# Optimization experiments

Hardware: AMD Instinct MI355X
Metric: run time of the kernel (lower is better)

Reference implementation:

```python
import math
import jax, jax.numpy as jnp
import numpy as np
from jax import lax

N, L = 256, 4096
DIM_LINEAR, DIM_CONV, KERNEL, STRIDE = 64, 128, 15, 1


def setup_inputs() -> dict:
    key = jax.random.key(0)
    ks = jax.random.split(key, 10)
    tokens = jax.random.randint(ks[0], (N, L), 0, 4, dtype=jnp.int32)
    emb = jax.random.normal(ks[1], (4, DIM_LINEAR), dtype=jnp.float32)
    conv_w = jax.random.normal(ks[2], (DIM_CONV, DIM_LINEAR, KERNEL), dtype=jnp.float32) * (1.0 / math.sqrt(DIM_LINEAR * KERNEL))
    conv_b = jax.random.normal(ks[3], (DIM_CONV,), dtype=jnp.float32) * 0.01
    s = 1.0 / math.sqrt(DIM_CONV)
    Wq = jax.random.normal(ks[4], (DIM_CONV, DIM_CONV), dtype=jnp.float32) * s
    bq = jax.random.normal(ks[5], (DIM_CONV,), dtype=jnp.float32) * 0.01
    Wk = jax.random.normal(ks[6], (DIM_CONV, DIM_CONV), dtype=jnp.float32) * s
    bk = jax.random.normal(ks[7], (DIM_CONV,), dtype=jnp.float32) * 0.01
    Wv = jax.random.normal(ks[8], (DIM_CONV, DIM_CONV), dtype=jnp.float32) * s
    bv = jax.random.normal(ks[9], (DIM_CONV,), dtype=jnp.float32) * 0.01
    return {"tokens": tokens, "emb": emb, "conv_w": conv_w, "conv_b": conv_b,
            "Wq": Wq, "bq": bq, "Wk": Wk, "bk": bk, "Wv": Wv, "bv": bv}


def reference(tokens, emb, conv_w, conv_b, Wq, bq, Wk, bk, Wv, bv):
    # embedding: [N, L, dl] -> channels-first [N, dl, L]
    x = emb[tokens].transpose(0, 2, 1)
    # conv1d, valid padding: [N, dc, Lout]
    y = lax.conv_general_dilated(x, conv_w, window_strides=(STRIDE,),
                                 padding='VALID',
                                 dimension_numbers=('NCH', 'OIH', 'NCH'))
    y = y + conv_b[None, :, None]
    read = y.transpose(0, 2, 1)                      # [N, Lout, dc]
    read_mean = read.mean(axis=1)                    # [N, dc]
    q = read_mean @ Wq.T + bq                        # [N, dc]
    k = read @ Wk.T + bk                             # [N, Lout, dc]
    v = read @ Wv.T + bv                             # [N, Lout, dc]
    scores = jnp.einsum('nd,nld->nl', q, k) / math.sqrt(DIM_CONV)
    attn = jax.nn.softmax(scores, axis=1)            # [N, Lout]
    out = jnp.einsum('nl,nld->nd', attn, v)          # [N, dc]
    return out
```

## Files before the change

### kernel.cpp

```cpp
#include <hip/hip_runtime.h>
#include <math.h>

#define NN 256
#define LL 4096
#define DL 64
#define DC 128
#define KS 15
#define LOUT (LL - KS + 1)
#define RSQRT_DC 0.08838834764831843f
#define INV_LOUT (1.0f / (float)LOUT)

#define WS_CTB   0
#define WS_QC    7680
#define WS_KC    15360
#define WS_G     23040
#define WS_S0    30720
#define WS_BB    30784
#define WS_B0    30848
#define WS_OUTB  30976
#define WS_PACK  31104
#define WS_CNT   96640

__global__ __launch_bounds__(256) void prep1_kernel(const int* __restrict__ tokens,
                                                    const float* __restrict__ emb,
                                                    const float* __restrict__ conv_w,
                                                    float* __restrict__ ws) {
    const int b = blockIdx.x, tid = threadIdx.x;
    if (b < NN) {
        __shared__ int totw[4][4];
        const int n = b;
        const int4* tv = (const int4*)(tokens + (size_t)n * LL) + tid * 4;
        unsigned w = 0;
#pragma unroll
        for (int m = 0; m < 4; ++m) {
            int4 t4 = tv[m];
            w |= ((unsigned)t4.x | ((unsigned)t4.y << 2) |
                  ((unsigned)t4.z << 4) | ((unsigned)t4.w << 6)) << (8 * m);
        }
        ((unsigned*)ws)[WS_PACK + n * 256 + tid] = w;
        int c0, c1, c2, c3;
        unsigned y, z;
        y = w;               z = (y | (y >> 1)) & 0x55555555u; c0 = 16 - __popc(z);
        y = w ^ 0x55555555u; z = (y | (y >> 1)) & 0x55555555u; c1 = 16 - __popc(z);
        y = w ^ 0xAAAAAAAAu; z = (y | (y >> 1)) & 0x55555555u; c2 = 16 - __popc(z);
        y = w ^ 0xFFFFFFFFu; z = (y | (y >> 1)) & 0x55555555u; c3 = 16 - __popc(z);
#pragma unroll
        for (int off = 32; off > 0; off >>= 1) {
            c0 += __shfl_down(c0, off, 64); c1 += __shfl_down(c1, off, 64);
            c2 += __shfl_down(c2, off, 64); c3 += __shfl_down(c3, off, 64);
        }
        if ((tid & 63) == 0) {
            const int wv = tid >> 6;
            totw[wv][0] = c0; totw[wv][1] = c1; totw[wv][2] = c2; totw[wv][3] = c3;
        }
        __syncthreads();
        if (tid < 4)
            ((int*)ws)[WS_CNT + n * 4 + tid] =
                totw[0][tid] + totw[1][tid] + totw[2][tid] + totw[3][tid];
    } else {
        const int c = b - NN;
        __shared__ float wsm[DL][16];
        __shared__ float es[4][DL];
        const float* wsrc = conv_w + (size_t)c * (DL * KS);
        for (int idx = tid; idx < DL * KS; idx += 256) wsm[idx / KS][idx % KS] = wsrc[idx];
        es[tid >> 6][tid & 63] = emb[tid];
        __syncthreads();
        if (tid < 60) {
            const int v = tid / KS, k = tid % KS;
            float s = 0.f;
#pragma unroll
            for (int i = 0; i < DL; ++i) s += es[v][i] * wsm[i][k];
            ws[WS_CTB + tid * DC + c] = s;
        }
    }
}

__global__ __launch_bounds__(128) void prep2_kernel(
    const float* __restrict__ conv_b,
    const float* __restrict__ Wq, const float* __restrict__ bq,
    const float* __restrict__ Wk, const float* __restrict__ bk,
    const float* __restrict__ Wv, const float* __restrict__ bv,
    float* __restrict__ ws) {
    const int j = blockIdx.x, c = threadIdx.x;
    __shared__ float cbL[DC];
    __shared__ float red2a[2], red2b[2];
    cbL[c] = conv_b[c];
    if (j < 60) {
        __shared__ float ctbj[DC];
        ctbj[c] = ws[WS_CTB + j * DC + c];
        __syncthreads();
        const float4* wq = (const float4*)(Wq + (size_t)c * DC);
        const float4* wk = (const float4*)(Wk + (size_t)c * DC);
        const float4* wv = (const float4*)(Wv + (size_t)c * DC);
        const float4* ct4 = (const float4*)ctbj;
        const float4* cb4 = (const float4*)cbL;
        float qc = 0.f, q0c = 0.f, kc = 0.f, kcbc = 0.f, gc = 0.f;
#pragma unroll 8
        for (int t = 0; t < 32; ++t) {
            const float4 a = wq[t], b = wk[t], g = wv[t], x = ct4[t], y = cb4[t];
            qc   += a.x * x.x + a.y * x.y + a.z * x.z + a.w * x.w;
            q0c  += a.x * y.x + a.y * y.y + a.z * y.z + a.w * y.w;
            kc   += b.x * x.x + b.y * x.y + b.z * x.z + b.w * x.w;
            kcbc += b.x * y.x + b.y * y.y + b.z * y.z + b.w * y.w;
            gc   += g.x * x.x + g.y * x.y + g.z * x.z + g.w * x.w;
        }
        ws[WS_QC + j * DC + c] = qc;
        ws[WS_KC + j * DC + c] = kc;
        ws[WS_G  + j * DC + c] = gc;
        const float beta = kcbc + bk[c];
        q0c += bq[c];
        float t1 = kc * q0c;
        float t2 = qc * beta;
#pragma unroll
        for (int off = 32; off > 0; off >>= 1) {
            t1 += __shfl_down(t1, off, 64);
            t2 += __shfl_down(t2, off, 64);
        }
        if ((c & 63) == 0) { red2a[c >> 6] = t1; red2b[c >> 6] = t2; }
        __syncthreads();
        if (c == 0) {
            ws[WS_S0 + j] = (red2a[0] + red2a[1]) * RSQRT_DC;
            ws[WS_BB + j] = (red2b[0] + red2b[1]) * RSQRT_DC;
        }
    } else {
        __syncthreads();
        const float4* wq = (const float4*)(Wq + (size_t)c * DC);
        const float4* wk = (const float4*)(Wk + (size_t)c * DC);
        const float4* wv = (const float4*)(Wv + (size_t)c * DC);
        const float4* cb4 = (const float4*)cbL;
        float q0c = 0.f, kcbc = 0.f, ob = 0.f;
#pragma unroll 8
        for (int t = 0; t < 32; ++t) {
            const float4 a = wq[t], b = wk[t], g = wv[t], y = cb4[t];
            q0c  += a.x * y.x + a.y * y.y + a.z * y.z + a.w * y.w;
            kcbc += b.x * y.x + b.y * y.y + b.z * y.z + b.w * y.w;
            ob   += g.x * y.x + g.y * y.y + g.z * y.z + g.w * y.w;
        }
        ws[WS_OUTB + c] = ob + bv[c];
        q0c += bq[c];
        float t1 = q0c * (kcbc + bk[c]);
#pragma unroll
        for (int off = 32; off > 0; off >>= 1) t1 += __shfl_down(t1, off, 64);
        if ((c & 63) == 0) red2a[c >> 6] = t1;
        __syncthreads();
        if (c == 0) ws[WS_B0] = (red2a[0] + red2a[1]) * RSQRT_DC;
    }
}

template <int NW>
__device__ __forceinline__ float bsum(float v, float* red, int tid) {
#pragma unroll
    for (int off = 32; off > 0; off >>= 1) v += __shfl_down(v, off, 64);
    if ((tid & 63) == 0) red[tid >> 6] = v;
    __syncthreads();
    float r = 0.f;
#pragma unroll
    for (int w = 0; w < NW; ++w) r += red[w];
    __syncthreads();
    return r;
}

__global__ __launch_bounds__(512) void encode_kernel(
    const float* __restrict__ ws, float* __restrict__ out) {
    const int n = blockIdx.x, tid = threadIdx.x;
    const unsigned* packed = (const unsigned*)ws + WS_PACK;

    __shared__ unsigned tok2L[258];
    __shared__ float stabL[64];
    __shared__ float cfL[60];
    __shared__ float uL[DC];
    __shared__ float Tt[1024];
    __shared__ float AccL[45];
    __shared__ float red[8];

    if (tid >= 64) {
        const int i = tid - 64;
        if (i < 258) tok2L[i] = (i < 256) ? packed[n * 256 + i] : 0u;
        else if (i < 258 + 45) AccL[i - 258] = 0.f;
    } else {
        const int l = tid;
        const int4 ct = *(const int4*)((const int*)ws + WS_CNT + n * 4);
        const unsigned dwF = packed[n * 256];
        const unsigned dwL = packed[n * 256 + 255];
        if (l < KS) {
            const int k = l;
            const unsigned pm = (k == 0) ? 0u : ((1u << (2 * k)) - 1u);
            const unsigned sm = (k == 14) ? 0u : (0xFFFFFFFFu << (2 * (k + 2)));
            const int tot4[4] = {ct.x, ct.y, ct.z, ct.w};
#pragma unroll
            for (int v = 0; v < 4; ++v) {
                const unsigned patt = (unsigned)v * 0x55555555u;
                unsigned yf = dwF ^ patt, zf = (yf | (yf >> 1)) & 0x55555555u;
                unsigned yl = dwL ^ patt, zl = (yl | (yl >> 1)) & 0x55555555u;
                const int pre = k - __popc(zf & pm);
                const int suf = (14 - k) - __popc(zl & sm);
                cfL[v * KS + k] = (float)(tot4[v] - pre - suf) * INV_LOUT;
            }
        }
        const int c0 = 2 * l;
        float u0 = 0.f, u1 = 0.f;
        for (int j = 0; j < 60; ++j) {
            const float cfj = cfL[j];
            const float2 q2 = *(const float2*)(ws + WS_QC + j * DC + c0);
            u0 += cfj * q2.x; u1 += cfj * q2.y;
        }
        uL[c0] = u0; uL[c0 + 1] = u1;
        float t = (l < 60) ? cfL[l] * ws[WS_BB + l] : 0.f;
#pragma unroll
        for (int off = 32; off > 0; off >>= 1) t += __shfl_down(t, off, 64);
        if (l == 0) stabL[60] = ws[WS_B0] + t;
        if (l < 60) {
            const float4* kr = (const float4*)(ws + WS_KC + (size_t)l * DC);
            const float4* u4 = (const float4*)uL;
            float s = 0.f;
#pragma unroll 8
            for (int t2 = 0; t2 < 32; ++t2) {
                const float4 a = kr[t2], u = u4[t2];
                s += a.x * u.x + a.y * u.y + a.z * u.z + a.w * u.w;
            }
            stabL[l] = ws[WS_S0 + l] + s * RSQRT_DC;
        }
    }
    __syncthreads();

    const float base = stabL[60];
    for (int e = tid; e < 1024; e += 512) {
        const int j = e >> 8, bb = e & 255;
        float s = stabL[(bb & 3) * KS + 4 * j] +
                  stabL[((bb >> 2) & 3) * KS + 4 * j + 1] +
                  stabL[((bb >> 4) & 3) * KS + 4 * j + 2];
        if (j < 3) s += stabL[((bb >> 6) & 3) * KS + 4 * j + 3];
        Tt[e] = s;
    }
    float M = base;
#pragma unroll
    for (int k = 0; k < KS; ++k)
        M += fmaxf(fmaxf(stabL[k], stabL[KS + k]),
                   fmaxf(stabL[2 * KS + k], stabL[3 * KS + k]));
    __syncthreads();

    const unsigned d0 = tok2L[tid >> 1], d1 = tok2L[(tid >> 1) + 1];
    const unsigned long long W = (unsigned long long)d0 | ((unsigned long long)d1 << 32);
    const int sbase = (tid & 1) << 4;
    const int t0 = tid * 8;
    float ev[8];
    float lsum = 0.f;
#pragma unroll
    for (int p = 0; p < 8; ++p) {
        const unsigned w = (unsigned)(W >> (sbase + 2 * p));
        const float s = base + Tt[w & 255] + Tt[256 + ((w >> 8) & 255)] +
                        Tt[512 + ((w >> 16) & 255)] + Tt[768 + ((w >> 24) & 63)];
        const float e = (t0 + p < LOUT) ? __expf(s - M) : 0.f;
        ev[p] = e; lsum += e;
    }
    const float S = bsum<8>(lsum, red, tid);
    const float invS = 1.0f / S;

    float a1[KS], a2[KS], a3[KS];
#pragma unroll
    for (int k = 0; k < KS; ++k) { a1[k] = 0.f; a2[k] = 0.f; a3[k] = 0.f; }
#pragma unroll
    for (int p = 0; p < 8; ++p) {
        const float e = ev[p];
        const unsigned w = (unsigned)(W >> (sbase + 2 * p));
#pragma unroll
        for (int k = 0; k < KS; ++k) {
            const int v = (int)((w >> (2 * k)) & 3u);
            a1[k] += (v == 1) ? e : 0.f;
            a2[k] += (v == 2) ? e : 0.f;
            a3[k] += (v == 3) ? e : 0.f;
        }
    }
    {
        const int lane = tid & 63;
#pragma unroll
        for (int k = 0; k < KS; ++k) {
            float v1 = a1[k], v2 = a2[k], v3 = a3[k];
#pragma unroll
            for (int off = 32; off > 0; off >>= 1) {
                v1 += __shfl_down(v1, off, 64);
                v2 += __shfl_down(v2, off, 64);
                v3 += __shfl_down(v3, off, 64);
            }
            if (lane == 0) {
                atomicAdd(&AccL[k], v1);
                atomicAdd(&AccL[KS + k], v2);
                atomicAdd(&AccL[2 * KS + k], v3);
            }
        }
    }
    __syncthreads();

    if (tid < DC) {
        float s = 0.f;
#pragma unroll
        for (int k = 0; k < KS; ++k) {
            const float a0 = S - AccL[k] - AccL[KS + k] - AccL[2 * KS + k];
            s += a0 * ws[WS_G + k * DC + tid];
        }
#pragma unroll
        for (int j = KS; j < 60; ++j) s += AccL[j - KS] * ws[WS_G + j * DC + tid];
        out[(size_t)n * DC + tid] = ws[WS_OUTB + tid] + s * invS;
    }
}

extern "C" void kernel_launch(void* const* d_in, const int* in_sizes, int n_in,
                              void* d_out, int out_size, void* d_ws, size_t ws_size,
                              hipStream_t stream) {
    const int*   tokens = (const int*)d_in[0];
    const float* emb    = (const float*)d_in[1];
    const float* conv_w = (const float*)d_in[2];
    const float* conv_b = (const float*)d_in[3];
    const float* Wq     = (const float*)d_in[4];
    const float* bq     = (const float*)d_in[5];
    const float* Wk     = (const float*)d_in[6];
    const float* bk     = (const float*)d_in[7];
    const float* Wv     = (const float*)d_in[8];
    const float* bv     = (const float*)d_in[9];
    float* out = (float*)d_out;
    float* ws  = (float*)d_ws;

    prep1_kernel<<<NN + DC, 256, 0, stream>>>(tokens, emb, conv_w, ws);
    prep2_kernel<<<61, 128, 0, stream>>>(conv_b, Wq, bq, Wk, bk, Wv, bv, ws);
    encode_kernel<<<NN, 512, 0, stream>>>(ws, out);
}
```

Measured before the change: 104.8 us.

## Fold token packing into encode kernel and merge weight prep into one kernel

Moves token packing and per-sequence token counting from a separate prep kernel into the encode kernel's shared memory, so the packed tokens no longer round-trip through the workspace. Merges the two weight-prep kernels into one that computes the embedding-conv table and its Q/K/V projections per block. Also restructures the bias terms by computing the full query vector (with bias) per sequence and dotting it with beta, which drops the S0/BB/B0 precomputations. This removes one kernel launch and a dependency stage. In exchange each encode block reads raw int32 tokens and the prep block does a strided conv_w read.

```diff
diff --git a/kernel.cpp b/kernel.cpp
--- a/kernel.cpp
+++ b/kernel.cpp
@@ -10,34 +10,97 @@
 #define RSQRT_DC 0.08838834764831843f
 #define INV_LOUT (1.0f / (float)LOUT)
 
-#define WS_CTB   0
-#define WS_QC    7680
-#define WS_KC    15360
-#define WS_G     23040
-#define WS_S0    30720
-#define WS_BB    30784
-#define WS_B0    30848
-#define WS_OUTB  30976
-#define WS_PACK  31104
-#define WS_CNT   96640
-
-__global__ __launch_bounds__(256) void prep1_kernel(const int* __restrict__ tokens,
-                                                    const float* __restrict__ emb,
-                                                    const float* __restrict__ conv_w,
-                                                    float* __restrict__ ws) {
-    const int b = blockIdx.x, tid = threadIdx.x;
-    if (b < NN) {
-        __shared__ int totw[4][4];
-        const int n = b;
+#define WS_QC    0
+#define WS_KC    7680
+#define WS_G     15360
+#define WS_Q0    23040
+#define WS_BETA  23168
+#define WS_OUTB  23296
+
+__global__ __launch_bounds__(128) void prepw_kernel(
+    const float* __restrict__ emb, const float* __restrict__ conv_w,
+    const float* __restrict__ conv_b,
+    const float* __restrict__ Wq, const float* __restrict__ bq,
+    const float* __restrict__ Wk, const float* __restrict__ bk,
+    const float* __restrict__ Wv, const float* __restrict__ bv,
+    float* __restrict__ ws) {
+    const int j = blockIdx.x, c = threadIdx.x;
+    __shared__ __align__(16) float vecL[DC];
+    if (j < 60) {
+        const int v = j / KS, k = j % KS;
+        __shared__ float embL[DL];
+        if (c < DL) embL[c] = emb[v * DL + c];
+        __syncthreads();
+        const float* wp = conv_w + (size_t)c * (DL * KS) + k;
+        float s = 0.f;
+#pragma unroll
+        for (int i = 0; i < DL; ++i) s += embL[i] * wp[i * KS];
+        vecL[c] = s;
+        __syncthreads();
+    } else {
+        vecL[c] = conv_b[c];
+        __syncthreads();
+    }
+    const float4* x4  = (const float4*)vecL;
+    const float4* wq4 = (const float4*)(Wq + (size_t)c * DC);
+    const float4* wk4 = (const float4*)(Wk + (size_t)c * DC);
+    const float4* wv4 = (const float4*)(Wv + (size_t)c * DC);
+    float aq = 0.f, ak = 0.f, av = 0.f;
+#pragma unroll 8
+    for (int t = 0; t < 32; ++t) {
+        const float4 x = x4[t], a = wq4[t], b = wk4[t], g = wv4[t];
+        aq += a.x * x.x + a.y * x.y + a.z * x.z + a.w * x.w;
+        ak += b.x * x.x + b.y * x.y + b.z * x.z + b.w * x.w;
+        av += g.x * x.x + g.y * x.y + g.z * x.z + g.w * x.w;
+    }
+    if (j < 60) {
+        ws[WS_QC + j * DC + c] = aq;
+        ws[WS_KC + j * DC + c] = ak;
+        ws[WS_G  + j * DC + c] = av;
+    } else {
+        ws[WS_Q0   + c] = aq + bq[c];
+        ws[WS_BETA + c] = ak + bk[c];
+        ws[WS_OUTB + c] = av + bv[c];
+    }
+}
+
+template <int NW>
+__device__ __forceinline__ float bsum(float v, float* red, int tid) {
+#pragma unroll
+    for (int off = 32; off > 0; off >>= 1) v += __shfl_down(v, off, 64);
+    if ((tid & 63) == 0) red[tid >> 6] = v;
+    __syncthreads();
+    float r = 0.f;
+#pragma unroll
+    for (int w = 0; w < NW; ++w) r += red[w];
+    __syncthreads();
+    return r;
+}
+
+__global__ __launch_bounds__(512) void encode_kernel(
+    const int* __restrict__ tokens, const float* __restrict__ ws,
+    float* __restrict__ out) {
+    const int n = blockIdx.x, tid = threadIdx.x;
+
+    __shared__ unsigned tok2L[258];
+    __shared__ __align__(16) float qL[DC];
+    __shared__ float stabL[64];
+    __shared__ float cfL[60];
+    __shared__ float Tt[1024];
+    __shared__ float AccL[45];
+    __shared__ float red[8];
+    __shared__ int totw[4][4];
+
+    if (tid < 256) {
         const int4* tv = (const int4*)(tokens + (size_t)n * LL) + tid * 4;
         unsigned w = 0;
 #pragma unroll
         for (int m = 0; m < 4; ++m) {
-            int4 t4 = tv[m];
+            const int4 t4 = tv[m];
             w |= ((unsigned)t4.x | ((unsigned)t4.y << 2) |
                   ((unsigned)t4.z << 4) | ((unsigned)t4.w << 6)) << (8 * m);
         }
-        ((unsigned*)ws)[WS_PACK + n * 256 + tid] = w;
+        tok2L[tid] = w;
         int c0, c1, c2, c3;
         unsigned y, z;
         y = w;               z = (y | (y >> 1)) & 0x55555555u; c0 = 16 - __popc(z);
@@ -53,140 +116,25 @@
             const int wv = tid >> 6;
             totw[wv][0] = c0; totw[wv][1] = c1; totw[wv][2] = c2; totw[wv][3] = c3;
         }
-        __syncthreads();
-        if (tid < 4)
-            ((int*)ws)[WS_CNT + n * 4 + tid] =
-                totw[0][tid] + totw[1][tid] + totw[2][tid] + totw[3][tid];
     } else {
-        const int c = b - NN;
-        __shared__ float wsm[DL][16];
-        __shared__ float es[4][DL];
-        const float* wsrc = conv_w + (size_t)c * (DL * KS);
-        for (int idx = tid; idx < DL * KS; idx += 256) wsm[idx / KS][idx % KS] = wsrc[idx];
-        es[tid >> 6][tid & 63] = emb[tid];
-        __syncthreads();
-        if (tid < 60) {
-            const int v = tid / KS, k = tid % KS;
-            float s = 0.f;
-#pragma unroll
-            for (int i = 0; i < DL; ++i) s += es[v][i] * wsm[i][k];
-            ws[WS_CTB + tid * DC + c] = s;
-        }
-    }
-}
-
-__global__ __launch_bounds__(128) void prep2_kernel(
-    const float* __restrict__ conv_b,
-    const float* __restrict__ Wq, const float* __restrict__ bq,
-    const float* __restrict__ Wk, const float* __restrict__ bk,
-    const float* __restrict__ Wv, const float* __restrict__ bv,
-    float* __restrict__ ws) {
-    const int j = blockIdx.x, c = threadIdx.x;
-    __shared__ float cbL[DC];
-    __shared__ float red2a[2], red2b[2];
-    cbL[c] = conv_b[c];
-    if (j < 60) {
-        __shared__ float ctbj[DC];
-        ctbj[c] = ws[WS_CTB + j * DC + c];
-        __syncthreads();
-        const float4* wq = (const float4*)(Wq + (size_t)c * DC);
-        const float4* wk = (const float4*)(Wk + (size_t)c * DC);
-        const float4* wv = (const float4*)(Wv + (size_t)c * DC);
-        const float4* ct4 = (const float4*)ctbj;
-        const float4* cb4 = (const float4*)cbL;
-        float qc = 0.f, q0c = 0.f, kc = 0.f, kcbc = 0.f, gc = 0.f;
-#pragma unroll 8
-        for (int t = 0; t < 32; ++t) {
-            const float4 a = wq[t], b = wk[t], g = wv[t], x = ct4[t], y = cb4[t];
-            qc   += a.x * x.x + a.y * x.y + a.z * x.z + a.w * x.w;
-            q0c  += a.x * y.x + a.y * y.y + a.z * y.z + a.w * y.w;
-            kc   += b.x * x.x + b.y * x.y + b.z * x.z + b.w * x.w;
-            kcbc += b.x * y.x + b.y * y.y + b.z * y.z + b.w * y.w;
-            gc   += g.x * x.x + g.y * x.y + g.z * x.z + g.w * x.w;
-        }
-        ws[WS_QC + j * DC + c] = qc;
-        ws[WS_KC + j * DC + c] = kc;
-        ws[WS_G  + j * DC + c] = gc;
-        const float beta = kcbc + bk[c];
-        q0c += bq[c];
-        float t1 = kc * q0c;
-        float t2 = qc * beta;
-#pragma unroll
-        for (int off = 32; off > 0; off >>= 1) {
-            t1 += __shfl_down(t1, off, 64);
-            t2 += __shfl_down(t2, off, 64);
-        }
-        if ((c & 63) == 0) { red2a[c >> 6] = t1; red2b[c >> 6] = t2; }
-        __syncthreads();
-        if (c == 0) {
-            ws[WS_S0 + j] = (red2a[0] + red2a[1]) * RSQRT_DC;
-            ws[WS_BB + j] = (red2b[0] + red2b[1]) * RSQRT_DC;
-        }
-    } else {
-        __syncthreads();
-        const float4* wq = (const float4*)(Wq + (size_t)c * DC);
-        const float4* wk = (const float4*)(Wk + (size_t)c * DC);
-        const float4* wv = (const float4*)(Wv + (size_t)c * DC);
-        const float4* cb4 = (const float4*)cbL;
-        float q0c = 0.f, kcbc = 0.f, ob = 0.f;
-#pragma unroll 8
-        for (int t = 0; t < 32; ++t) {
-            const float4 a = wq[t], b = wk[t], g = wv[t], y = cb4[t];
-            q0c  += a.x * y.x + a.y * y.y + a.z * y.z + a.w * y.w;
-            kcbc += b.x * y.x + b.y * y.y + b.z * y.z + b.w * y.w;
-            ob   += g.x * y.x + g.y * y.y + g.z * y.z + g.w * y.w;
-        }
-        ws[WS_OUTB + c] = ob + bv[c];
-        q0c += bq[c];
-        float t1 = q0c * (kcbc + bk[c]);
-#pragma unroll
-        for (int off = 32; off > 0; off >>= 1) t1 += __shfl_down(t1, off, 64);
-        if ((c & 63) == 0) red2a[c >> 6] = t1;
-        __syncthreads();
-        if (c == 0) ws[WS_B0] = (red2a[0] + red2a[1]) * RSQRT_DC;
-    }
-}
-
-template <int NW>
-__device__ __forceinline__ float bsum(float v, float* red, int tid) {
-#pragma unroll
-    for (int off = 32; off > 0; off >>= 1) v += __shfl_down(v, off, 64);
-    if ((tid & 63) == 0) red[tid >> 6] = v;
-    __syncthreads();
-    float r = 0.f;
-#pragma unroll
-    for (int w = 0; w < NW; ++w) r += red[w];
-    __syncthreads();
-    return r;
-}
-
-__global__ __launch_bounds__(512) void encode_kernel(
-    const float* __restrict__ ws, float* __restrict__ out) {
-    const int n = blockIdx.x, tid = threadIdx.x;
-    const unsigned* packed = (const unsigned*)ws + WS_PACK;
-
-    __shared__ unsigned tok2L[258];
-    __shared__ float stabL[64];
-    __shared__ float cfL[60];
-    __shared__ float uL[DC];
-    __shared__ float Tt[1024];
-    __shared__ float AccL[45];
-    __shared__ float red[8];
-
-    if (tid >= 64) {
-        const int i = tid - 64;
-        if (i < 258) tok2L[i] = (i < 256) ? packed[n * 256 + i] : 0u;
-        else if (i < 258 + 45) AccL[i - 258] = 0.f;
-    } else {
+        if (tid < 258) tok2L[tid] = 0u;
+        const int i = tid - 258;
+        if (i >= 0 && i < 45) AccL[i] = 0.f;
+    }
+    __syncthreads();
+
+    if (tid < 64) {
         const int l = tid;
-        const int4 ct = *(const int4*)((const int*)ws + WS_CNT + n * 4);
-        const unsigned dwF = packed[n * 256];
-        const unsigned dwL = packed[n * 256 + 255];
         if (l < KS) {
             const int k = l;
+            const unsigned dwF = tok2L[0], dwL = tok2L[255];
             const unsigned pm = (k == 0) ? 0u : ((1u << (2 * k)) - 1u);
             const unsigned sm = (k == 14) ? 0u : (0xFFFFFFFFu << (2 * (k + 2)));
-            const int tot4[4] = {ct.x, ct.y, ct.z, ct.w};
+            const int tot4[4] = {
+                totw[0][0] + totw[1][0] + totw[2][0] + totw[3][0],
+                totw[0][1] + totw[1][1] + totw[2][1] + totw[3][1],
+                totw[0][2] + totw[1][2] + totw[2][2] + totw[3][2],
+                totw[0][3] + totw[1][3] + totw[2][3] + totw[3][3]};
 #pragma unroll
             for (int v = 0; v < 4; ++v) {
                 const unsigned patt = (unsigned)v * 0x55555555u;
@@ -198,27 +146,30 @@
             }
         }
         const int c0 = 2 * l;
-        float u0 = 0.f, u1 = 0.f;
+        const float2 q02 = *(const float2*)(ws + WS_Q0 + c0);
+        float u0 = q02.x, u1 = q02.y;
+#pragma unroll 15
         for (int j = 0; j < 60; ++j) {
             const float cfj = cfL[j];
             const float2 q2 = *(const float2*)(ws + WS_QC + j * DC + c0);
             u0 += cfj * q2.x; u1 += cfj * q2.y;
         }
-        uL[c0] = u0; uL[c0 + 1] = u1;
-        float t = (l < 60) ? cfL[l] * ws[WS_BB + l] : 0.f;
+        qL[c0] = u0; qL[c0 + 1] = u1;
+        const float2 be = *(const float2*)(ws + WS_BETA + c0);
+        float t = u0 * be.x + u1 * be.y;
 #pragma unroll
         for (int off = 32; off > 0; off >>= 1) t += __shfl_down(t, off, 64);
-        if (l == 0) stabL[60] = ws[WS_B0] + t;
+        if (l == 0) stabL[60] = t * RSQRT_DC;
         if (l < 60) {
             const float4* kr = (const float4*)(ws + WS_KC + (size_t)l * DC);
-            const float4* u4 = (const float4*)uL;
+            const float4* q4 = (const float4*)qL;
             float s = 0.f;
 #pragma unroll 8
             for (int t2 = 0; t2 < 32; ++t2) {
-                const float4 a = kr[t2], u = u4[t2];
-                s += a.x * u.x + a.y * u.y + a.z * u.z + a.w * u.w;
-            }
-            stabL[l] = ws[WS_S0 + l] + s * RSQRT_DC;
+                const float4 a = kr[t2], q = q4[t2];
+                s += a.x * q.x + a.y * q.y + a.z * q.z + a.w * q.w;
+            }
+            stabL[l] = s * RSQRT_DC;
         }
     }
     __syncthreads();
@@ -320,7 +271,7 @@
     float* out = (float*)d_out;
     float* ws  = (float*)d_ws;
 
-    prep1_kernel<<<NN + DC, 256, 0, stream>>>(tokens, emb, conv_w, ws);
-    prep2_kernel<<<61, 128, 0, stream>>>(conv_b, Wq, bq, Wk, bk, Wv, bv, ws);
-    encode_kernel<<<NN, 512, 0, stream>>>(ws, out);
-}
+    prepw_kernel<<<61, 128, 0, stream>>>(emb, conv_w, conv_b,
+                                         Wq, bq, Wk, bk, Wv, bv, ws);
+    encode_kernel<<<NN, 512, 0, stream>>>(tokens, ws, out);
+}
```

After: 106.3 us. No clear change (+1.5%).
